# Performance work log

Measured on AMD Instinct MI355X. Metric: run time of the kernel, lower is better.

Reference implementation:

```python
import jax, jax.numpy as jnp
import numpy as np

OUT_SIZE = 7          # pooled output H=W
SPATIAL_SCALE = 0.125 # FPN stride 8
SAMPLE_NUM = 2        # sampling grid per bin (static)
N_ORIENT = 8
PI = 3.141592653589793


def setup_inputs() -> dict:
    key = jax.random.key(0)
    k1, k2, k3, k4, k5 = jax.random.split(key, 5)
    features = jax.random.normal(k1, (2, 256, 256, 256), dtype=jnp.float32)
    R = 512
    batch = jax.random.randint(k2, (R,), 0, 2).astype(jnp.float32)
    centers = jax.random.uniform(k3, (R, 2), minval=64.0, maxval=1984.0)
    wh = jax.random.uniform(k4, (R, 2), minval=32.0, maxval=512.0)
    theta = jax.random.uniform(k5, (R, 1), minval=0.0, maxval=2.0 * PI)
    rois = jnp.concatenate([batch[:, None], centers, wh, theta], axis=1)
    return {"features": features, "rois": rois}


def _riroi_align(features, rois):
    B, Ctot, H, W = features.shape
    O = N_ORIENT
    C = Ctot // O
    P, G = OUT_SIZE, SAMPLE_NUM
    dtype = features.dtype
    Rn = rois.shape[0]

    batch_ind = rois[:, 0].astype(jnp.int32)
    cw = rois[:, 1] * SPATIAL_SCALE
    ch = rois[:, 2] * SPATIAL_SCALE
    rw = jnp.maximum(rois[:, 3] * SPATIAL_SCALE, 1.0)
    rh = jnp.maximum(rois[:, 4] * SPATIAL_SCALE, 1.0)
    theta = rois[:, 5]

    # orientation alignment: interpolate between two circularly-shifted channels
    ind_f = theta * O / (2.0 * PI)
    ind_floor = jnp.floor(ind_f)
    l_var = ind_f - ind_floor          # weight on shifted-plus-one plane
    r_var = 1.0 - l_var
    ind = jnp.mod(ind_floor.astype(jnp.int32), O)
    o_idx = jnp.arange(O, dtype=jnp.int32)
    ind_rot = jnp.mod(o_idx[None, :] - ind[:, None], O)   # [R,O]
    ind_rot_p = jnp.mod(ind_rot + 1, O)

    # rotated sampling grid; layout (ph, iy, pw, ix) flattened to S
    bin_h = rh / P
    bin_w = rw / P
    pidx = jnp.arange(P, dtype=dtype)
    gidx = (jnp.arange(G, dtype=dtype) + 0.5) / G
    yy = -rh[:, None, None] / 2.0 + (pidx[None, :, None] + gidx[None, None, :]) * bin_h[:, None, None]  # [R,P,G]
    xx = -rw[:, None, None] / 2.0 + (pidx[None, :, None] + gidx[None, None, :]) * bin_w[:, None, None]
    yy = yy[:, :, :, None, None]          # [R,P,G,1,1]
    xx = xx[:, None, None, :, :]          # [R,1,1,P,G]
    cos_t = jnp.cos(theta)[:, None, None, None, None]
    sin_t = jnp.sin(theta)[:, None, None, None, None]
    x = (xx * cos_t - yy * sin_t + cw[:, None, None, None, None]).reshape(Rn, -1)  # [R,S]
    y = (xx * sin_t + yy * cos_t + ch[:, None, None, None, None]).reshape(Rn, -1)
    S = x.shape[1]

    # bilinear interpolation corner indices/weights (ROIAlign semantics)
    valid = (y > -1.0) & (y < H) & (x > -1.0) & (x < W)
    yc = jnp.clip(y, 0.0, None)
    xc = jnp.clip(x, 0.0, None)
    y_low = yc.astype(jnp.int32)
    x_low = xc.astype(jnp.int32)
    y_edge = y_low >= H - 1
    x_edge = x_low >= W - 1
    y_high = jnp.where(y_edge, H - 1, y_low + 1)
    x_high = jnp.where(x_edge, W - 1, x_low + 1)
    y_low = jnp.where(y_edge, H - 1, y_low)
    x_low = jnp.where(x_edge, W - 1, x_low)
    yv = jnp.where(y_edge, y_low.astype(dtype), yc)
    xv = jnp.where(x_edge, x_low.astype(dtype), xc)
    ly = yv - y_low.astype(dtype)
    lx = xv - x_low.astype(dtype)
    hy = 1.0 - ly
    hx = 1.0 - lx
    vm = valid.astype(dtype)
    w00 = hy * hx * vm
    w01 = hy * lx * vm
    w10 = ly * hx * vm
    w11 = ly * lx * vm

    # [B,O,H,W,C] so the channel dim is gathered contiguously
    feats = features.reshape(B, C, O, H, W).transpose(0, 2, 3, 4, 1)
    b = batch_ind[:, None, None]  # [R,1,1]
    yl = y_low[:, None, :]
    yh = y_high[:, None, :]
    xl = x_low[:, None, :]
    xh = x_high[:, None, :]

    def gather_plane(plane):  # plane [R,O] -> [R,O,S,C]
        p = plane[:, :, None]
        return (w00[:, None, :, None] * feats[b, p, yl, xl]
                + w01[:, None, :, None] * feats[b, p, yl, xh]
                + w10[:, None, :, None] * feats[b, p, yh, xl]
                + w11[:, None, :, None] * feats[b, p, yh, xh])

    val = gather_plane(ind_rot)
    val_p = gather_plane(ind_rot_p)
    out = r_var[:, None, None, None] * val + l_var[:, None, None, None] * val_p  # [R,O,S,C]
    out = out.reshape(Rn, O, P, G, P, G, C).mean(axis=(3, 5))  # average over bin samples
    out = out.transpose(0, 4, 1, 2, 3).reshape(Rn, C * O, P, P)  # channel layout c*O + o
    return out


def reference(features, rois):
    return _riroi_align(features, rois)
```

## Files before the change

### kernel.cpp

```cpp
#include <hip/hip_runtime.h>
#include <hip/hip_fp16.h>


typedef _Float16 h16;
typedef _Float16 h8 __attribute__((ext_vector_type(8)));

#define NS 196
#define HW 65536
#define TWO_PI_F 6.283185307179586f
#define OPITCH 132
#define TP 40

__global__ __launch_bounds__(256) void transpose_kernel(
    const float* __restrict__ in, h16* __restrict__ out)
{
    __shared__ h16 lds[256 * TP];
    const int t = threadIdx.x;
    const int a = t & 63;
    const int w = t >> 6;

    const int b  = blockIdx.z;
    const int tc = blockIdx.y;
    const int tp = blockIdx.x;

    const float* ip = in + ((size_t)b * 256 + tc * 32 + w * 8) * HW + tp * 256 + a * 4;

    float4 v[8];
    #pragma unroll
    for (int j = 0; j < 8; ++j)
        v[j] = *(const float4*)(ip + (size_t)j * HW);

    #pragma unroll
    for (int p = 0; p < 4; ++p) {
        h8 row;
        #pragma unroll
        for (int j = 0; j < 8; ++j)
            row[j] = (h16)(((const float*)&v[j])[p]);
        *(h8*)&lds[(a * 4 + p) * TP + w * 8] = row;
    }
    __syncthreads();

    h16* op = out + ((size_t)b * HW + (size_t)tp * 256) * 256 + tc * 32;
    #pragma unroll
    for (int k = 0; k < 4; ++k) {
        int px   = (t >> 2) + k * 64;
        int part = t & 3;
        h8 r = *(const h8*)&lds[px * TP + part * 8];
        *(h8*)(op + (size_t)px * 256 + part * 8) = r;
    }
}

__global__ __launch_bounds__(512, 8) void riroi_gather(
    const h16* __restrict__ ft, const float* __restrict__ rois,
    float* __restrict__ out)
{
    const int r    = blockIdx.x >> 1;
    const int half = blockIdx.x & 1;
    const int tid  = threadIdx.x;
    const int lane = tid & 63;
    const int wave = tid >> 6;
    const int cn   = lane >> 4;
    const int chg  = lane & 15;

    const float* roi = rois + r * 6;
    const int   b  = (int)roi[0];
    const float cw = roi[1] * 0.125f;
    const float ch = roi[2] * 0.125f;
    const float rw = fmaxf(roi[3] * 0.125f, 1.0f);
    const float rh = fmaxf(roi[4] * 0.125f, 1.0f);
    const float theta = roi[5];

    const float ind_f = theta * 8.0f / TWO_PI_F;
    const float fl    = floorf(ind_f);
    const float lvar  = ind_f - fl;
    const float rvar  = 1.0f - lvar;
    int ii = (int)fl;
    const int ind = ((ii % 8) + 8) & 7;

    const float cost = cosf(theta), sint = sinf(theta);
    const float bin_h = rh / 7.0f, bin_w = rw / 7.0f;

    __shared__ int   s_off[4][NS];
    __shared__ float s_w[4][NS];
    __shared__ float s_out[49 * OPITCH];

    if (tid < NS) {
        int iy = tid / 14, ix = tid - iy * 14;
        int py = iy >> 1, gy = iy & 1;
        int px = ix >> 1, gx = ix & 1;
        float yy = ((float)py + ((float)gy + 0.5f) * 0.5f) * bin_h - rh * 0.5f;
        float xx = ((float)px + ((float)gx + 0.5f) * 0.5f) * bin_w - rw * 0.5f;
        float x = xx * cost - yy * sint + cw;
        float y = xx * sint + yy * cost + ch;
        float vm = (y > -1.0f && y < 256.0f && x > -1.0f && x < 256.0f) ? 1.0f : 0.0f;
        float yc = fmaxf(y, 0.0f), xc = fmaxf(x, 0.0f);
        int y0 = (int)yc, x0 = (int)xc;
        int y1, x1; float yv, xv;
        if (y0 >= 255) { y0 = 255; y1 = 255; yv = 255.0f; }
        else           { y1 = y0 + 1; yv = yc; }
        if (x0 >= 255) { x0 = 255; x1 = 255; xv = 255.0f; }
        else           { x1 = x0 + 1; xv = xc; }
        float ly = yv - (float)y0, lx = xv - (float)x0;
        float hy = 1.0f - ly, hx = 1.0f - lx;
        s_w[0][tid] = hy * hx * vm;
        s_w[1][tid] = hy * lx * vm;
        s_w[2][tid] = ly * hx * vm;
        s_w[3][tid] = ly * lx * vm;
        int y0w = y0 << 8, y1w = y1 << 8;
        s_off[0][tid] = (y0w + x0) << 8;
        s_off[1][tid] = (y0w + x1) << 8;
        s_off[2][tid] = (y1w + x0) << 8;
        s_off[3][tid] = (y1w + x1) << 8;
    }
    __syncthreads();

    const h16* fb = ft + (size_t)b * ((size_t)HW * 256) + half * 128 + (chg << 3);

    for (int bin = wave; bin < 49; bin += 8) {
        int py = bin / 7, px = bin - py * 7;
        int sbase = py * 28 + px * 2;
        float v[8] = {0.f, 0.f, 0.f, 0.f, 0.f, 0.f, 0.f, 0.f};
        #pragma unroll
        for (int k = 0; k < 4; ++k) {
            int   s   = sbase + (k & 1) + ((k & 2) ? 14 : 0);
            int   o   = s_off[cn][s];
            float wgt = s_w[cn][s];
            h8 f = *(const h8*)(fb + o);
            #pragma unroll
            for (int i = 0; i < 8; ++i)
                v[i] += wgt * (float)f[i];
        }
        #pragma unroll
        for (int i = 0; i < 8; ++i) {
            v[i] += __shfl_xor(v[i], 16);
            v[i] += __shfl_xor(v[i], 32);
        }
        if (cn == 0) {
            float res[8];
            #pragma unroll
            for (int i = 0; i < 8; ++i)
                res[i] = 0.25f * (rvar * v[i] + lvar * v[(i + 1) & 7]);
            float* dst = &s_out[bin * OPITCH + (chg << 3)];
            *(float4*)dst       = make_float4(res[0], res[1], res[2], res[3]);
            *(float4*)(dst + 4) = make_float4(res[4], res[5], res[6], res[7]);
        }
    }
    __syncthreads();

    const int ind_neg = (8 - ind) & 7;
    float* ob = out + (size_t)r * 12544 + half * 6272;
    for (int i = tid << 2; i < 6272; i += 2048) {
        float4 vo;
        #pragma unroll
        for (int q = 0; q < 4; ++q) {
            int j   = i + q;
            int co  = j / 49;
            int bin = j - co * 49;
            int ci  = (co & ~7) | ((co + ind_neg) & 7);
            ((float*)&vo)[q] = s_out[bin * OPITCH + ci];
        }
        *(float4*)(ob + i) = vo;
    }
}

extern "C" void kernel_launch(void* const* d_in, const int* in_sizes, int n_in,
                              void* d_out, int out_size, void* d_ws, size_t ws_size,
                              hipStream_t stream) {
    const float* feat = (const float*)d_in[0];
    const float* rois = (const float*)d_in[1];
    float* out = (float*)d_out;

    h16* ft = (h16*)d_ws;
    transpose_kernel<<<dim3(256, 8, 2), dim3(256), 0, stream>>>(feat, ft);
    riroi_gather<<<dim3(1024), dim3(512), 0, stream>>>(ft, rois, out);
}
```

Before: 248.2 us.

## Assign one bin per 16-lane group and drop cross-lane shuffle reduction

Sampling offsets and weights are stored per bin as contiguous int4/float4 groups, so each 16-lane quarter-wave handles a whole bin on its own: all 16 corner loads in a loop, accumulated locally. This removes the xor-shuffle reduction and the idle-lane writeback, and raises loads in flight per thread. The batch index and orientation shift are forced scalar with readfirstlane, and divide-by-7 becomes a multiply. In exchange each thread holds more registers, and the second pass leaves part of the wave idle.

```diff
diff --git a/kernel.cpp b/kernel.cpp
--- a/kernel.cpp
+++ b/kernel.cpp
@@ -59,11 +59,11 @@
     const int tid  = threadIdx.x;
     const int lane = tid & 63;
     const int wave = tid >> 6;
-    const int cn   = lane >> 4;
+    const int bq   = lane >> 4;
     const int chg  = lane & 15;
 
     const float* roi = rois + r * 6;
-    const int   b  = (int)roi[0];
+    int bb = (int)roi[0];
     const float cw = roi[1] * 0.125f;
     const float ch = roi[2] * 0.125f;
     const float rw = fmaxf(roi[3] * 0.125f, 1.0f);
@@ -75,19 +75,24 @@
     const float lvar  = ind_f - fl;
     const float rvar  = 1.0f - lvar;
     int ii = (int)fl;
-    const int ind = ((ii % 8) + 8) & 7;
+    int ind_v = ((ii % 8) + 8) & 7;
+    const int b   = __builtin_amdgcn_readfirstlane(bb);
+    const int ind = __builtin_amdgcn_readfirstlane(ind_v);
 
     const float cost = cosf(theta), sint = sinf(theta);
-    const float bin_h = rh / 7.0f, bin_w = rw / 7.0f;
+    const float bin_h = rh * (1.0f / 7.0f), bin_w = rw * (1.0f / 7.0f);
 
-    __shared__ int   s_off[4][NS];
-    __shared__ float s_w[4][NS];
+    __shared__ int   s_off[49 * 16];
+    __shared__ float s_w  [49 * 16];
     __shared__ float s_out[49 * OPITCH];
 
     if (tid < NS) {
         int iy = tid / 14, ix = tid - iy * 14;
         int py = iy >> 1, gy = iy & 1;
         int px = ix >> 1, gx = ix & 1;
+        int bin  = py * 7 + px;
+        int slot = (gy << 1) | gx;
+        int base = (bin << 4) + (slot << 2);
         float yy = ((float)py + ((float)gy + 0.5f) * 0.5f) * bin_h - rh * 0.5f;
         float xx = ((float)px + ((float)gx + 0.5f) * 0.5f) * bin_w - rw * 0.5f;
         float x = xx * cost - yy * sint + cw;
@@ -102,40 +107,35 @@
         else           { x1 = x0 + 1; xv = xc; }
         float ly = yv - (float)y0, lx = xv - (float)x0;
         float hy = 1.0f - ly, hx = 1.0f - lx;
-        s_w[0][tid] = hy * hx * vm;
-        s_w[1][tid] = hy * lx * vm;
-        s_w[2][tid] = ly * hx * vm;
-        s_w[3][tid] = ly * lx * vm;
         int y0w = y0 << 8, y1w = y1 << 8;
-        s_off[0][tid] = (y0w + x0) << 8;
-        s_off[1][tid] = (y0w + x1) << 8;
-        s_off[2][tid] = (y1w + x0) << 8;
-        s_off[3][tid] = (y1w + x1) << 8;
+        *(int4*)&s_off[base] = make_int4((y0w + x0) << 8, (y0w + x1) << 8,
+                                         (y1w + x0) << 8, (y1w + x1) << 8);
+        *(float4*)&s_w[base] = make_float4(hy * hx * vm, hy * lx * vm,
+                                           ly * hx * vm, ly * lx * vm);
     }
     __syncthreads();
 
     const h16* fb = ft + (size_t)b * ((size_t)HW * 256) + half * 128 + (chg << 3);
 
-    for (int bin = wave; bin < 49; bin += 8) {
-        int py = bin / 7, px = bin - py * 7;
-        int sbase = py * 28 + px * 2;
-        float v[8] = {0.f, 0.f, 0.f, 0.f, 0.f, 0.f, 0.f, 0.f};
-        #pragma unroll
-        for (int k = 0; k < 4; ++k) {
-            int   s   = sbase + (k & 1) + ((k & 2) ? 14 : 0);
-            int   o   = s_off[cn][s];
-            float wgt = s_w[cn][s];
-            h8 f = *(const h8*)(fb + o);
+    #pragma unroll
+    for (int pass = 0; pass < 2; ++pass) {
+        const int bin = pass * 32 + (wave << 2) + bq;
+        if (bin < 49) {
+            const int dbase = bin << 4;
+            float v[8] = {0.f, 0.f, 0.f, 0.f, 0.f, 0.f, 0.f, 0.f};
             #pragma unroll
-            for (int i = 0; i < 8; ++i)
-                v[i] += wgt * (float)f[i];
-        }
-        #pragma unroll
-        for (int i = 0; i < 8; ++i) {
-            v[i] += __shfl_xor(v[i], 16);
-            v[i] += __shfl_xor(v[i], 32);
-        }
-        if (cn == 0) {
+            for (int s = 0; s < 4; ++s) {
+                int4   o = *(const int4*)  &s_off[dbase + (s << 2)];
+                float4 w = *(const float4*)&s_w  [dbase + (s << 2)];
+                h8 f0 = *(const h8*)(fb + o.x);
+                h8 f1 = *(const h8*)(fb + o.y);
+                h8 f2 = *(const h8*)(fb + o.z);
+                h8 f3 = *(const h8*)(fb + o.w);
+                #pragma unroll
+                for (int i = 0; i < 8; ++i)
+                    v[i] += w.x * (float)f0[i] + w.y * (float)f1[i]
+                          + w.z * (float)f2[i] + w.w * (float)f3[i];
+            }
             float res[8];
             #pragma unroll
             for (int i = 0; i < 8; ++i)
```

After: 302.0 us. +21.7%, slower.
